# Optimization experiments

Hardware: AMD Instinct MI355X
Metric: run time of the kernel (lower is better)

## Reference

```python
import jax, jax.numpy as jnp
import numpy as np

D_MODEL = 1024
N_HEADS = 16
D_K = D_MODEL // N_HEADS
EPS = 1e-6


def setup_inputs() -> dict:
    key = jax.random.key(0)
    ks = jax.random.split(key, 9)
    s = 1.0 / np.sqrt(D_MODEL)
    x = jax.random.normal(ks[0], (4, 4096, D_MODEL), dtype=jnp.float32)
    Wq = jax.random.uniform(ks[1], (D_MODEL, D_MODEL), jnp.float32, -s, s)
    bq = jax.random.uniform(ks[2], (D_MODEL,), jnp.float32, -s, s)
    Wk = jax.random.uniform(ks[3], (D_MODEL, D_MODEL), jnp.float32, -s, s)
    bk = jax.random.uniform(ks[4], (D_MODEL,), jnp.float32, -s, s)
    Wv = jax.random.uniform(ks[5], (D_MODEL, D_MODEL), jnp.float32, -s, s)
    bv = jax.random.uniform(ks[6], (D_MODEL,), jnp.float32, -s, s)
    Wo = jax.random.uniform(ks[7], (D_MODEL, D_MODEL), jnp.float32, -s, s)
    bo = jax.random.uniform(ks[8], (D_MODEL,), jnp.float32, -s, s)
    return {"x": x, "Wq": Wq, "bq": bq, "Wk": Wk, "bk": bk,
            "Wv": Wv, "bv": bv, "Wo": Wo, "bo": bo}


def _feature_map(t):
    # elu(x) + 1
    return jax.nn.elu(t) + 1.0


def reference(x, Wq, bq, Wk, bk, Wv, bv, Wo, bo):
    b, s, _ = x.shape
    # projections, split into heads: [b, h, s, d_k]
    def heads(t):
        return t.reshape(b, s, N_HEADS, D_K).transpose(0, 2, 1, 3)
    q = _feature_map(heads(x @ Wq + bq))
    k = _feature_map(heads(x @ Wk + bk))
    v = heads(x @ Wv + bv)
    # kv accumulation: [b, h, d_k, d_k]
    kv = jnp.einsum('bhsd,bhse->bhde', k, v)
    # normalizer: q . sum_s k  -> [b, h, s, 1]
    z = jnp.einsum('bhsd,bhd->bhs', q, k.sum(axis=2))[..., None]
    out = jnp.einsum('bhsd,bhde->bhse', q, kv) / (z + EPS)
    out = out.transpose(0, 2, 1, 3).reshape(b, s, D_MODEL)
    return out @ Wo + bo
```

## Files before the change

kernel.cpp:

```cpp
#include <hip/hip_runtime.h>


typedef __bf16 bf16;
typedef float  f32x4  __attribute__((ext_vector_type(4)));
typedef short  s16x8  __attribute__((ext_vector_type(8)));
typedef bf16   bf16x4 __attribute__((ext_vector_type(4)));

#define BATCH 4
#define SEQ   4096
#define DM    1024
#define NH    16
#define DK    64
#define MROWS (BATCH*SEQ)
#define EPSV  1e-6f
#define NXB   (MROWS*DM/1024)

__device__ __forceinline__ void async_cp16(const bf16* g, bf16* l) {
  __builtin_amdgcn_global_load_lds((const __attribute__((address_space(1))) void*)g,
                                   (__attribute__((address_space(3))) void*)l,
                                   16, 0, 0);
}

__global__ __launch_bounds__(256) void conv_fused_kernel(const float* __restrict__ x,
                                                         bf16* __restrict__ xb,
                                                         const float* __restrict__ W0,
                                                         const float* __restrict__ W1,
                                                         const float* __restrict__ W2,
                                                         const float* __restrict__ W3,
                                                         bf16* __restrict__ Wt) {
  __shared__ bf16 tt[64][72];
  const int bid = blockIdx.x;
  const int tid = threadIdx.x;
  if (bid < NXB) {
    int i = (bid * 256 + tid) * 4;
    float4 f = *reinterpret_cast<const float4*>(x + i);
    bf16x4 o;
    o[0] = (bf16)f.x; o[1] = (bf16)f.y; o[2] = (bf16)f.z; o[3] = (bf16)f.w;
    *reinterpret_cast<bf16x4*>(xb + i) = o;
    return;
  }
  const int b2 = bid - NXB;
  const int z = b2 >> 8;
  const float* W = (z == 0) ? W0 : (z == 1) ? W1 : (z == 2) ? W2 : W3;
  const int n0 = (b2 & 15) * 64, k0 = ((b2 >> 4) & 15) * 64;
#pragma unroll
  for (int i = 0; i < 4; ++i) {
    const int c = tid + i * 256;
    const int krow = c >> 4, nch = c & 15;
    float4 f = *reinterpret_cast<const float4*>(W + (size_t)(k0 + krow) * DM + n0 + nch * 4);
    tt[nch * 4 + 0][krow] = (bf16)f.x;
    tt[nch * 4 + 1][krow] = (bf16)f.y;
    tt[nch * 4 + 2][krow] = (bf16)f.z;
    tt[nch * 4 + 3][krow] = (bf16)f.w;
  }
  __syncthreads();
#pragma unroll
  for (int i = 0; i < 2; ++i) {
    const int c = tid + i * 256;
    const int nrow = c >> 3, kch = c & 7;
    *reinterpret_cast<uint4*>(Wt + (size_t)(z * DM + n0 + nrow) * DM + k0 + kch * 8) =
        *reinterpret_cast<const uint4*>(&tt[nrow][kch * 8]);
  }
}

template <int MODE>
__global__ __launch_bounds__(512, 2) void gemm_bf16(const bf16* __restrict__ A,
                                                    const bf16* __restrict__ Bt,
                                                    void* __restrict__ Cout, int ldc,
                                                    const float* __restrict__ b0,
                                                    const float* __restrict__ b1,
                                                    const float* __restrict__ b2,
                                                    bf16* __restrict__ kt,
                                                    bf16* __restrict__ vt) {
  constexpr int K  = 1024;
  constexpr int BK = 64;
  constexpr int NT = K / BK;
  __shared__ __align__(16) char smem[131072];

  const int tid  = threadIdx.x;
  const int wv   = tid >> 6, lane = tid & 63;
  const int quad = lane >> 4, l16 = lane & 15;
  const int swk  = l16 & 7;

  const int w = blockIdx.y * gridDim.x + blockIdx.x;
  const int j = w >> 3;
  const int bm0 = (((w & 7) << 3) + (j & 7)) << 8;
  const int bn0 = (j >> 3) << 8;

  const int wm = wv >> 2;
  const int wn = wv & 3;

  f32x4 acc[8][4] = {};
  s16x8 af[4][2];
  s16x8 bq[2][2][2];

  const int srow = wv * 8 + (lane >> 3);
  const int scol = ((lane & 7) ^ (lane >> 3)) * 8;
  const bf16* Ag = A  + (size_t)(bm0 + srow) * K + scol;
  const bf16* Bg = Bt + (size_t)(bn0 + srow) * K + scol;
  const int sbase = wv * 1024;

#define STAGE_A(t_, h_) do {                                                   \
    const bf16* g_ = Ag + (size_t)((h_) * 128) * K + (t_) * BK;                \
    char* l_ = smem + ((t_) & 1) * 32768 + (h_) * 16384 + sbase;               \
    async_cp16(g_, (bf16*)l_);                                                 \
    async_cp16(g_ + (size_t)64 * K, (bf16*)(l_ + 8192));                       \
  } while (0)
#define STAGE_B(t_, h_) do {                                                   \
    const bf16* g_ = Bg + (size_t)((h_) * 128) * K + (t_) * BK;                \
    char* l_ = smem + 65536 + ((t_) & 1) * 32768 + (h_) * 16384 + sbase;       \
    async_cp16(g_, (bf16*)l_);                                                 \
    async_cp16(g_ + (size_t)64 * K, (bf16*)(l_ + 8192));                       \
  } while (0)
#define LDA(pb_, qm_) do {                                                     \
    const char* ab_ = smem + (pb_) * 32768 +                                   \
        (size_t)(wm * 128 + (qm_) * 64 + l16) * 128;                           \
    _Pragma("unroll") for (int mi = 0; mi < 4; ++mi)                           \
      _Pragma("unroll") for (int ks = 0; ks < 2; ++ks)                         \
        af[mi][ks] = *reinterpret_cast<const s16x8*>(                          \
            ab_ + mi * 2048 + (((ks * 4 + quad) ^ swk) << 4));                 \
  } while (0)
#define LDB(pb_, qn_) do {                                                     \
    const char* bb_ = smem + 65536 + (pb_) * 32768 +                           \
        (size_t)(wn * 64 + (qn_) * 32 + l16) * 128;                            \
    _Pragma("unroll") for (int ni = 0; ni < 2; ++ni)                           \
      _Pragma("unroll") for (int ks = 0; ks < 2; ++ks)                         \
        bq[qn_][ni][ks] = *reinterpret_cast<const s16x8*>(                     \
            bb_ + ni * 2048 + (((ks * 4 + quad) ^ swk) << 4));                 \
  } while (0)
#define MFMA_Q(qm_, qn_) do {                                                  \
    _Pragma("unroll") for (int mi = 0; mi < 4; ++mi)                           \
      _Pragma("unroll") for (int ni = 0; ni < 2; ++ni)                         \
        _Pragma("unroll") for (int ks = 0; ks < 2; ++ks)                       \
          acc[(qm_) * 4 + mi][(qn_) * 2 + ni] =                                \
              __builtin_amdgcn_mfma_f32_16x16x32_bf16(                         \
                  af[mi][ks], bq[qn_][ni][ks],                                 \
                  acc[(qm_) * 4 + mi][(qn_) * 2 + ni], 0, 0, 0);               \
  } while (0)

  STAGE_B(0, 0); STAGE_A(0, 0); STAGE_B(0, 1); STAGE_A(0, 1);
  STAGE_B(1, 0); STAGE_A(1, 0);
  asm volatile("s_waitcnt vmcnt(4)");
  __builtin_amdgcn_s_barrier();
  __builtin_amdgcn_sched_barrier(0);
  LDA(0, 0); LDB(0, 0); LDB(0, 1);
  __builtin_amdgcn_sched_barrier(0);

#pragma unroll 2
  for (int t = 0; t < NT; ++t) {
    const int p = t & 1;
    if (t + 1 < NT) STAGE_B(t + 1, 1);
    asm volatile("s_waitcnt lgkmcnt(0)");
    __builtin_amdgcn_sched_barrier(0);
    __builtin_amdgcn_s_setprio(1);
    MFMA_Q(0, 0); MFMA_Q(0, 1);
    __builtin_amdgcn_s_setprio(0);
    LDA(p, 1);
    __builtin_amdgcn_sched_barrier(0);
    if (t + 1 < NT) STAGE_A(t + 1, 1);
    asm volatile("s_waitcnt lgkmcnt(0)");
    __builtin_amdgcn_sched_barrier(0);
    __builtin_amdgcn_s_setprio(1);
    MFMA_Q(1, 0); MFMA_Q(1, 1);
    __builtin_amdgcn_s_setprio(0);
    __builtin_amdgcn_s_barrier();
    __builtin_amdgcn_sched_barrier(0);
    if (t + 2 < NT) { STAGE_B(t + 2, 0); STAGE_A(t + 2, 0); }
    if (t + 1 < NT) {
      if (t + 2 < NT) asm volatile("s_waitcnt vmcnt(4)");
      else            asm volatile("s_waitcnt vmcnt(0)");
      __builtin_amdgcn_s_barrier();
      __builtin_amdgcn_sched_barrier(0);
      LDA(p ^ 1, 0); LDB(p ^ 1, 0); LDB(p ^ 1, 1);
      __builtin_amdgcn_sched_barrier(0);
    }
  }

  if (MODE == 0) {
    const int part = bn0 >> 10;
    if (part == 0) {
      bf16* C = (bf16*)Cout;
      bf16 (*Cw)[64] = (bf16(*)[64])(smem + wv * 16384);
#pragma unroll
      for (int ni = 0; ni < 4; ++ni) {
        const int n_l = ni * 16 + l16;
        const float bias = b0[bn0 + wn * 64 + n_l];
#pragma unroll
        for (int mi = 0; mi < 8; ++mi)
#pragma unroll
          for (int r = 0; r < 4; ++r) {
            float v = acc[mi][ni][r] + bias;
            v = (v > 0.f) ? (v + 1.f) : __expf(v);
            const int row = mi * 16 + quad * 4 + r;
            Cw[row][n_l ^ ((row & 7) << 3)] = (bf16)v;
          }
      }
#pragma unroll
      for (int i = 0; i < 16; ++i) {
        const int row = i * 8 + (lane >> 3), ch = lane & 7;
        *reinterpret_cast<uint4*>(C + (size_t)(bm0 + wm * 128 + row) * ldc +
                                  bn0 + wn * 64 + ch * 8) =
            *reinterpret_cast<const uint4*>(&Cw[row][(ch ^ (row & 7)) * 8]);
      }
    } else {
      bf16* T = (part == 1) ? kt : vt;
      const float* bp = (part == 1) ? b1 : b2;
      const int b  = bm0 >> 12;
      const int h  = ((bn0 & 1023) >> 6) + wn;
      const int s_loc = (bm0 & 4095) + wm * 128;
      bf16* base = T + (size_t)(b * 16 + h) * 64 * 4096 + s_loc;
      char* sl = smem + wv * 16384;
#pragma unroll
      for (int ni = 0; ni < 4; ++ni) {
        const int d = ni * 16 + l16;
        const float bias = bp[(bn0 + wn * 64 + d) & 1023];
#pragma unroll
        for (int mi = 0; mi < 8; ++mi) {
          bf16x4 o;
#pragma unroll
          for (int r = 0; r < 4; ++r) {
            float v = acc[mi][ni][r] + bias;
            if (part == 1) v = (v > 0.f) ? (v + 1.f) : __expf(v);
            o[r] = (bf16)v;
          }
          const int sb = mi * 32 + quad * 8;
          *reinterpret_cast<uint2*>(sl + d * 256 + (sb ^ ((d & 7) << 4))) =
              *reinterpret_cast<const uint2*>(&o);
        }
      }
#pragma unroll
      for (int i = 0; i < 16; ++i) {
        const int d = i * 4 + (lane >> 4), ch = l16;
        const uint4 val = *reinterpret_cast<const uint4*>(
            sl + d * 256 + ((ch * 16) ^ ((d & 7) << 4)));
        *reinterpret_cast<uint4*>(base + (size_t)d * 4096 + ch * 8) = val;
      }
    }
  } else {
    float* C = (float*)Cout;
    float (*Cwf)[64] = (float(*)[64])(smem + wv * 16384);
#pragma unroll
    for (int h = 0; h < 2; ++h) {
#pragma unroll
      for (int ni = 0; ni < 4; ++ni) {
        const int n_l = ni * 16 + l16;
        const float bias = b0[bn0 + wn * 64 + n_l];
#pragma unroll
        for (int mi = 0; mi < 4; ++mi)
#pragma unroll
          for (int r = 0; r < 4; ++r) {
            const int row = mi * 16 + quad * 4 + r;
            Cwf[row][n_l ^ ((row & 7) << 2)] = acc[h * 4 + mi][ni][r] + bias;
          }
      }
#pragma unroll
      for (int i = 0; i < 16; ++i) {
        const int row = i * 4 + (lane >> 4), ch = lane & 15;
        *reinterpret_cast<float4*>(C + (size_t)(bm0 + wm * 128 + h * 64 + row) * ldc +
                                   bn0 + wn * 64 + ch * 4) =
            *reinterpret_cast<const float4*>(&Cwf[row][(ch ^ (row & 7)) * 4]);
      }
    }
  }
#undef STAGE_A
#undef STAGE_B
#undef LDA
#undef LDB
#undef MFMA_Q
}

__global__ __launch_bounds__(256) void kvk_mfma_kernel(const bf16* __restrict__ KT,
                                                       const bf16* __restrict__ VT,
                                                       float* __restrict__ kvT,
                                                       float* __restrict__ ksum) {
  __shared__ bf16 Ks[64][136];
  __shared__ bf16 Vs[64][136];
  __shared__ float red[4][4096];
  const int bh = blockIdx.y;
  const int tid = threadIdx.x;
  const int wv = tid >> 6, lane = tid & 63;
  const int quad = lane >> 4, l16 = lane & 15;
  const size_t tb = (size_t)bh * 64 * 4096;
  const int s0b = blockIdx.x * 1024;

  f32x4 acc[4][4] = {};
  float ksp[4] = {};

  for (int cc = 0; cc < 8; ++cc) {
    const int s0 = s0b + cc * 128;
    __syncthreads();
#pragma unroll
    for (int i = 0; i < 4; ++i) {
      const int c = tid + i * 256;
      const int row = c >> 4, ch = c & 15;
      const size_t go = tb + (size_t)row * 4096 + s0 + ch * 8;
      uint4 kk = *reinterpret_cast<const uint4*>(KT + go);
      *reinterpret_cast<uint4*>(&Ks[row][ch * 8]) = kk;
      *reinterpret_cast<uint4*>(&Vs[row][ch * 8]) =
          *reinterpret_cast<const uint4*>(VT + go);
      const bf16* kp = reinterpret_cast<const bf16*>(&kk);
      float t = 0.f;
#pragma unroll
      for (int jj = 0; jj < 8; ++jj) t += (float)kp[jj];
      ksp[i] += t;
    }
    __syncthreads();
    const int kb = wv * 32 + quad * 8;
    s16x8 vfr[4], kfr[4];
#pragma unroll
    for (int mi = 0; mi < 4; ++mi) {
      vfr[mi] = *reinterpret_cast<const s16x8*>(&Vs[mi * 16 + l16][kb]);
      kfr[mi] = *reinterpret_cast<const s16x8*>(&Ks[mi * 16 + l16][kb]);
    }
#pragma unroll
    for (int mi = 0; mi < 4; ++mi)
#pragma unroll
      for (int ni = 0; ni < 4; ++ni)
        acc[mi][ni] = __builtin_amdgcn_mfma_f32_16x16x32_bf16(vfr[mi], kfr[ni],
                                                              acc[mi][ni], 0, 0, 0);
  }
#pragma unroll
  for (int mi = 0; mi < 4; ++mi)
#pragma unroll
    for (int ni = 0; ni < 4; ++ni)
#pragma unroll
      for (int r = 0; r < 4; ++r)
        red[wv][(mi * 16 + quad * 4 + r) * 64 + ni * 16 + l16] = acc[mi][ni][r];
  __syncthreads();
#pragma unroll
  for (int jj = 0; jj < 4; ++jj) {
    const int c0 = tid * 16 + jj * 4;
    const float4 s0 = *reinterpret_cast<const float4*>(&red[0][c0]);
    const float4 s1 = *reinterpret_cast<const float4*>(&red[1][c0]);
    const float4 s2 = *reinterpret_cast<const float4*>(&red[2][c0]);
    const float4 s3 = *reinterpret_cast<const float4*>(&red[3][c0]);
    atomicAdd(&kvT[tb / 64 + c0 + 0], s0.x + s1.x + s2.x + s3.x);
    atomicAdd(&kvT[tb / 64 + c0 + 1], s0.y + s1.y + s2.y + s3.y);
    atomicAdd(&kvT[tb / 64 + c0 + 2], s0.z + s1.z + s2.z + s3.z);
    atomicAdd(&kvT[tb / 64 + c0 + 3], s0.w + s1.w + s2.w + s3.w);
  }
#pragma unroll
  for (int i = 0; i < 4; ++i)
#pragma unroll
    for (int o = 8; o > 0; o >>= 1)
      ksp[i] += __shfl_down(ksp[i], o, 16);
  if (l16 == 0) {
    const int g = tid >> 4;
#pragma unroll
    for (int i = 0; i < 4; ++i)
      atomicAdd(&ksum[bh * 64 + g + 16 * i], ksp[i]);
  }
}

__global__ __launch_bounds__(256) void attn_kernel(const bf16* __restrict__ Qb,
                                                   const float* __restrict__ kvT,
                                                   const float* __restrict__ ksum,
                                                   bf16* __restrict__ ATT) {
  __shared__ bf16 qs[128][72];
  __shared__ bf16 kvs[64][72];
  __shared__ bf16 Ps[128][72];
  __shared__ float zr[128];
  __shared__ float kss[64];
  const int bh = blockIdx.y;
  const int b = bh >> 4, h = bh & 15;
  const int s0 = blockIdx.x * 128;
  const int tid = threadIdx.x, wave = tid >> 6, lane = tid & 63;
  const int quad = lane >> 4, l16 = lane & 15;
  const size_t base = (size_t)b * SEQ * DM;
  const int colQ = h * 64;

#pragma unroll
  for (int i = 0; i < 4; ++i) {
    const int c = tid + i * 256;
    const int row = c >> 3, off = (c & 7) * 8;
    *reinterpret_cast<uint4*>(&qs[row][off]) =
        *reinterpret_cast<const uint4*>(Qb + base + (size_t)(s0 + row) * DM + colQ + off);
  }
  const float* kvg = kvT + (size_t)bh * 4096;
#pragma unroll
  for (int i = 0; i < 4; ++i) {
    const int c = tid + i * 256;
    const int row = c >> 4, off = (c & 15) * 4;
    float4 f = *reinterpret_cast<const float4*>(kvg + row * 64 + off);
    bf16x4 o;
    o[0] = (bf16)f.x; o[1] = (bf16)f.y; o[2] = (bf16)f.z; o[3] = (bf16)f.w;
    *reinterpret_cast<bf16x4*>(&kvs[row][off]) = o;
  }
  if (tid < 64) kss[tid] = ksum[bh * 64 + tid];
  __syncthreads();

  if (tid < 128) {
    float z = 0.f;
#pragma unroll
    for (int d = 0; d < 64; d += 4) {
      bf16x4 q4 = *reinterpret_cast<const bf16x4*>(&qs[tid][d]);
      z += (float)q4[0] * kss[d] + (float)q4[1] * kss[d + 1] +
           (float)q4[2] * kss[d + 2] + (float)q4[3] * kss[d + 3];
    }
    zr[tid] = 1.0f / (z + EPSV);
  }
  __syncthreads();

  const int wn = wave * 32;
  f32x4 pacc[4][2] = {};
#pragma unroll
  for (int ks = 0; ks < 2; ++ks) {
    s16x8 af[4], bf2[2];
#pragma unroll
    for (int mi = 0; mi < 4; ++mi)
      af[mi] = *reinterpret_cast<const s16x8*>(&kvs[mi * 16 + l16][ks * 32 + quad * 8]);
#pragma unroll
    for (int ni = 0; ni < 2; ++ni)
      bf2[ni] = *reinterpret_cast<const s16x8*>(&qs[wn + ni * 16 + l16][ks * 32 + quad * 8]);
#pragma unroll
    for (int mi = 0; mi < 4; ++mi)
#pragma unroll
      for (int ni = 0; ni < 2; ++ni)
        pacc[mi][ni] = __builtin_amdgcn_mfma_f32_16x16x32_bf16(af[mi], bf2[ni],
                                                               pacc[mi][ni], 0, 0, 0);
  }
#pragma unroll
  for (int ni = 0; ni < 2; ++ni) {
    const int s = wn + ni * 16 + l16;
    const float zi = zr[s];
#pragma unroll
    for (int mi = 0; mi < 4; ++mi) {
      bf16x4 o;
#pragma unroll
      for (int r = 0; r < 4; ++r) o[r] = (bf16)(pacc[mi][ni][r] * zi);
      *reinterpret_cast<bf16x4*>(&Ps[s][mi * 16 + quad * 4]) = o;
    }
  }
  __syncthreads();
#pragma unroll
  for (int i = 0; i < 4; ++i) {
    const int c = tid + i * 256;
    const int row = c >> 3, ch = c & 7;
    *reinterpret_cast<uint4*>(ATT + ((size_t)b * SEQ + s0 + row) * DM + h * 64 + ch * 8) =
        *reinterpret_cast<const uint4*>(&Ps[row][ch * 8]);
  }
}

extern "C" void kernel_launch(void* const* d_in, const int* in_sizes, int n_in,
                              void* d_out, int out_size, void* d_ws, size_t ws_size,
                              hipStream_t stream) {
  const float* x  = (const float*)d_in[0];
  const float* Wq = (const float*)d_in[1];
  const float* bq = (const float*)d_in[2];
  const float* Wk = (const float*)d_in[3];
  const float* bk = (const float*)d_in[4];
  const float* Wv = (const float*)d_in[5];
  const float* bv = (const float*)d_in[6];
  const float* Wo = (const float*)d_in[7];
  const float* bo = (const float*)d_in[8];
  float* out = (float*)d_out;

  char* ws = (char*)d_ws;
  bf16*  Xb   = (bf16*)ws;   ws += (size_t)MROWS * DM * 2;
  bf16*  Wt   = (bf16*)ws;   ws += (size_t)4 * DM * DM * 2;
  bf16*  Qb   = (bf16*)ws;   ws += (size_t)MROWS * DM * 2;
  bf16*  KT   = (bf16*)ws;   ws += (size_t)64 * 64 * 4096 * 2;
  bf16*  VT   = (bf16*)ws;   ws += (size_t)64 * 64 * 4096 * 2;
  bf16*  ATT  = (bf16*)ws;   ws += (size_t)MROWS * DM * 2;
  float* kvT  = (float*)ws;  ws += (size_t)64 * 4096 * 4;
  float* ksum = (float*)ws;  ws += (size_t)64 * 64 * 4;

  (void)hipMemsetAsync(kvT, 0, (size_t)64 * 4096 * 4 + (size_t)64 * 64 * 4, stream);

  conv_fused_kernel<<<NXB + 1024, 256, 0, stream>>>(x, Xb, Wq, Wk, Wv, Wo, Wt);
  gemm_bf16<0><<<dim3(12, 64), 512, 0, stream>>>(Xb, Wt, Qb, DM, bq, bk, bv, KT, VT);
  kvk_mfma_kernel<<<dim3(4, 64), 256, 0, stream>>>(KT, VT, kvT, ksum);
  attn_kernel<<<dim3(32, 64), 256, 0, stream>>>(Qb, kvT, ksum, ATT);
  gemm_bf16<1><<<dim3(4, 64), 512, 0, stream>>>(ATT, Wt + (size_t)3 * DM * DM, out, DM,
                                                bo, bo, bo, nullptr, nullptr);
}
```

Before: 349.3 us.

## Replace kv atomics with per-split partial buffers and batch x conversion per thread

The kv/ksum reduction across the four sequence splits now writes separate partial buffers with plain vector stores instead of float atomics. The attention kernel sums the four partials itself when it loads kv and ksum. This removes the memset launch and the atomic traffic, at the cost of four times more reads in attn_kernel. Separately, the x-to-bf16 conversion uses 2048 blocks that each handle 8 float4 elements, instead of one block per 1024 elements, which shrinks the conversion grid.

```diff
diff --git a/kernel.cpp b/kernel.cpp
--- a/kernel.cpp
+++ b/kernel.cpp
@@ -13,7 +13,6 @@
 #define DK    64
 #define MROWS (BATCH*SEQ)
 #define EPSV  1e-6f
-#define NXB   (MROWS*DM/1024)
 
 __device__ __forceinline__ void async_cp16(const bf16* g, bf16* l) {
   __builtin_amdgcn_global_load_lds((const __attribute__((address_space(1))) void*)g,
@@ -31,15 +30,19 @@
   __shared__ bf16 tt[64][72];
   const int bid = blockIdx.x;
   const int tid = threadIdx.x;
-  if (bid < NXB) {
-    int i = (bid * 256 + tid) * 4;
-    float4 f = *reinterpret_cast<const float4*>(x + i);
-    bf16x4 o;
-    o[0] = (bf16)f.x; o[1] = (bf16)f.y; o[2] = (bf16)f.z; o[3] = (bf16)f.w;
-    *reinterpret_cast<bf16x4*>(xb + i) = o;
+  if (bid < 2048) {
+    const int base = bid * 256 + tid;
+#pragma unroll
+    for (int it = 0; it < 8; ++it) {
+      const int idx = base + it * 524288;
+      float4 f = *reinterpret_cast<const float4*>(x + (size_t)idx * 4);
+      bf16x4 o;
+      o[0] = (bf16)f.x; o[1] = (bf16)f.y; o[2] = (bf16)f.z; o[3] = (bf16)f.w;
+      *reinterpret_cast<bf16x4*>(xb + (size_t)idx * 4) = o;
+    }
     return;
   }
-  const int b2 = bid - NXB;
+  const int b2 = bid - 2048;
   const int z = b2 >> 8;
   const float* W = (z == 0) ? W0 : (z == 1) ? W1 : (z == 2) ? W2 : W3;
   const int n0 = (b2 & 15) * 64, k0 = ((b2 >> 4) & 15) * 64;
@@ -271,8 +274,8 @@
 
 __global__ __launch_bounds__(256) void kvk_mfma_kernel(const bf16* __restrict__ KT,
                                                        const bf16* __restrict__ VT,
-                                                       float* __restrict__ kvT,
-                                                       float* __restrict__ ksum) {
+                                                       float* __restrict__ kvT4,
+                                                       float* __restrict__ ksum4) {
   __shared__ bf16 Ks[64][136];
   __shared__ bf16 Vs[64][136];
   __shared__ float red[4][4096];
@@ -327,6 +330,7 @@
       for (int r = 0; r < 4; ++r)
         red[wv][(mi * 16 + quad * 4 + r) * 64 + ni * 16 + l16] = acc[mi][ni][r];
   __syncthreads();
+  float* outp = kvT4 + ((size_t)blockIdx.x * 64 + bh) * 4096;
 #pragma unroll
   for (int jj = 0; jj < 4; ++jj) {
     const int c0 = tid * 16 + jj * 4;
@@ -334,10 +338,12 @@
     const float4 s1 = *reinterpret_cast<const float4*>(&red[1][c0]);
     const float4 s2 = *reinterpret_cast<const float4*>(&red[2][c0]);
     const float4 s3 = *reinterpret_cast<const float4*>(&red[3][c0]);
-    atomicAdd(&kvT[tb / 64 + c0 + 0], s0.x + s1.x + s2.x + s3.x);
-    atomicAdd(&kvT[tb / 64 + c0 + 1], s0.y + s1.y + s2.y + s3.y);
-    atomicAdd(&kvT[tb / 64 + c0 + 2], s0.z + s1.z + s2.z + s3.z);
-    atomicAdd(&kvT[tb / 64 + c0 + 3], s0.w + s1.w + s2.w + s3.w);
+    float4 o;
+    o.x = s0.x + s1.x + s2.x + s3.x;
+    o.y = s0.y + s1.y + s2.y + s3.y;
+    o.z = s0.z + s1.z + s2.z + s3.z;
+    o.w = s0.w + s1.w + s2.w + s3.w;
+    *reinterpret_cast<float4*>(outp + c0) = o;
   }
 #pragma unroll
   for (int i = 0; i < 4; ++i)
@@ -348,13 +354,13 @@
     const int g = tid >> 4;
 #pragma unroll
     for (int i = 0; i < 4; ++i)
-      atomicAdd(&ksum[bh * 64 + g + 16 * i], ksp[i]);
+      ksum4[((size_t)blockIdx.x * 64 + bh) * 64 + g + 16 * i] = ksp[i];
   }
 }
 
 __global__ __launch_bounds__(256) void attn_kernel(const bf16* __restrict__ Qb,
-                                                   const float* __restrict__ kvT,
-                                                   const float* __restrict__ ksum,
+                                                   const float* __restrict__ kvT4,
+                                                   const float* __restrict__ ksum4,
                                                    bf16* __restrict__ ATT) {
   __shared__ bf16 qs[128][72];
   __shared__ bf16 kvs[64][72];
@@ -376,17 +382,27 @@
     *reinterpret_cast<uint4*>(&qs[row][off]) =
         *reinterpret_cast<const uint4*>(Qb + base + (size_t)(s0 + row) * DM + colQ + off);
   }
-  const float* kvg = kvT + (size_t)bh * 4096;
+  const float* kv0 = kvT4 + (size_t)bh * 4096;
 #pragma unroll
   for (int i = 0; i < 4; ++i) {
     const int c = tid + i * 256;
     const int row = c >> 4, off = (c & 15) * 4;
-    float4 f = *reinterpret_cast<const float4*>(kvg + row * 64 + off);
+    const int lin = row * 64 + off;
+    float4 f0 = *reinterpret_cast<const float4*>(kv0 + lin);
+    float4 f1 = *reinterpret_cast<const float4*>(kv0 + 64 * 4096 + lin);
+    float4 f2 = *reinterpret_cast<const float4*>(kv0 + 2 * 64 * 4096 + lin);
+    float4 f3 = *reinterpret_cast<const float4*>(kv0 + 3 * 64 * 4096 + lin);
     bf16x4 o;
-    o[0] = (bf16)f.x; o[1] = (bf16)f.y; o[2] = (bf16)f.z; o[3] = (bf16)f.w;
+    o[0] = (bf16)(f0.x + f1.x + f2.x + f3.x);
+    o[1] = (bf16)(f0.y + f1.y + f2.y + f3.y);
+    o[2] = (bf16)(f0.z + f1.z + f2.z + f3.z);
+    o[3] = (bf16)(f0.w + f1.w + f2.w + f3.w);
     *reinterpret_cast<bf16x4*>(&kvs[row][off]) = o;
   }
-  if (tid < 64) kss[tid] = ksum[bh * 64 + tid];
+  if (tid < 64) {
+    const float* ks0 = ksum4 + (size_t)bh * 64 + tid;
+    kss[tid] = ks0[0] + ks0[64 * 64] + ks0[2 * 64 * 64] + ks0[3 * 64 * 64];
+  }
   __syncthreads();
 
   if (tid < 128) {
@@ -462,15 +478,13 @@
   bf16*  KT   = (bf16*)ws;   ws += (size_t)64 * 64 * 4096 * 2;
   bf16*  VT   = (bf16*)ws;   ws += (size_t)64 * 64 * 4096 * 2;
   bf16*  ATT  = (bf16*)ws;   ws += (size_t)MROWS * DM * 2;
-  float* kvT  = (float*)ws;  ws += (size_t)64 * 4096 * 4;
-  float* ksum = (float*)ws;  ws += (size_t)64 * 64 * 4;
-
-  (void)hipMemsetAsync(kvT, 0, (size_t)64 * 4096 * 4 + (size_t)64 * 64 * 4, stream);
-
-  conv_fused_kernel<<<NXB + 1024, 256, 0, stream>>>(x, Xb, Wq, Wk, Wv, Wo, Wt);
+  float* kvT4 = (float*)ws;  ws += (size_t)4 * 64 * 4096 * 4;
+  float* ksum4= (float*)ws;  ws += (size_t)4 * 64 * 64 * 4;
+
+  conv_fused_kernel<<<3072, 256, 0, stream>>>(x, Xb, Wq, Wk, Wv, Wo, Wt);
   gemm_bf16<0><<<dim3(12, 64), 512, 0, stream>>>(Xb, Wt, Qb, DM, bq, bk, bv, KT, VT);
-  kvk_mfma_kernel<<<dim3(4, 64), 256, 0, stream>>>(KT, VT, kvT, ksum);
-  attn_kernel<<<dim3(32, 64), 256, 0, stream>>>(Qb, kvT, ksum, ATT);
+  kvk_mfma_kernel<<<dim3(4, 64), 256, 0, stream>>>(KT, VT, kvT4, ksum4);
+  attn_kernel<<<dim3(32, 64), 256, 0, stream>>>(Qb, kvT4, ksum4, ATT);
   gemm_bf16<1><<<dim3(4, 64), 512, 0, stream>>>(ATT, Wt + (size_t)3 * DM * DM, out, DM,
                                                 bo, bo, bo, nullptr, nullptr);
 }
```

New measurement: 314.0 us. 1.11x faster.
